# Optimization experiments

Hardware: AMD Instinct MI355X
Metric: run time of the kernel (lower is better)

Reference implementation:

```python
import jax, jax.numpy as jnp
import numpy as np

N_HEADS = 16
EMBED_DIM = 1024
HEAD_DIM = EMBED_DIM // N_HEADS
SRC_LEN = 128  # diagonal offset of the tril mask
B, T = 2, 2048


def setup_inputs() -> dict:
    key = jax.random.key(0)
    ks = jax.random.split(key, 7)
    s = 0.02
    return {
        "x": jax.random.normal(ks[0], (B, T, EMBED_DIM), dtype=jnp.float32),
        "Wq": jax.random.normal(ks[1], (EMBED_DIM, EMBED_DIM), dtype=jnp.float32) * s,
        "bq": jax.random.normal(ks[2], (EMBED_DIM,), dtype=jnp.float32) * s,
        "Wk": jax.random.normal(ks[3], (EMBED_DIM, EMBED_DIM), dtype=jnp.float32) * s,
        "bk": jax.random.normal(ks[4], (EMBED_DIM,), dtype=jnp.float32) * s,
        "Wv": jax.random.normal(ks[5], (EMBED_DIM, EMBED_DIM), dtype=jnp.float32) * s,
        "bv": jax.random.normal(ks[6], (EMBED_DIM,), dtype=jnp.float32) * s,
    }


def reference(x, Wq, bq, Wk, bk, Wv, bv):
    b, t, c = x.shape
    # project and split heads: [B, H, T, Dh]
    def heads(w, bias):
        y = x @ w.T + bias
        return y.reshape(b, t, N_HEADS, HEAD_DIM).transpose(0, 2, 1, 3)

    q = heads(Wq, bq)
    k = heads(Wk, bk)
    v = heads(Wv, bv)

    scale = HEAD_DIM ** -0.5
    attn = jnp.einsum("bhqd,bhkd->bhqk", q, k) * scale  # [B,H,T,T]
    # prefix-causal mask: key j allowed iff j <= i + SRC_LEN
    i = jnp.arange(t)[:, None]
    j = jnp.arange(t)[None, :]
    mask = j <= i + SRC_LEN  # [T, T]
    attn = jnp.where(mask[None, None], attn, -jnp.inf)
    attn = jax.nn.softmax(attn, axis=-1)
    # dropout p=0.0 -> identity in eval/reference
    out = jnp.einsum("bhqk,bhkd->bhqd", attn, v)  # [B,H,T,Dh]
    return out.transpose(0, 2, 1, 3).reshape(b, t, c)
```

## Files before the change

### kernel.cpp

```cpp
#include <hip/hip_runtime.h>
#include <hip/hip_bf16.h>

#define B_    2
#define T_    2048
#define C_    1024
#define H_    16
#define D_    64
#define SRCL_ 128

typedef short  short8 __attribute__((ext_vector_type(8)));
typedef float  f32x4  __attribute__((ext_vector_type(4)));
typedef unsigned short ushort4_t __attribute__((ext_vector_type(4)));

#define QSCALE 0.18033688011112042f

__device__ inline unsigned short f2bf(float f) {
    union { float f; unsigned u; } v; v.f = f;
    unsigned r = v.u + 0x7FFFu + ((v.u >> 16) & 1u);
    return (unsigned short)(r >> 16);
}

#if __has_builtin(__builtin_amdgcn_exp2f)
#define EXP2F(x) __builtin_amdgcn_exp2f(x)
#else
#define EXP2F(x) exp2f(x)
#endif

__device__ __forceinline__ void async_ld16(const void* g, void* l) {
    __builtin_amdgcn_global_load_lds(
        (const __attribute__((address_space(1))) unsigned int*)g,
        (__attribute__((address_space(3))) unsigned int*)l, 16, 0, 0);
}

__global__ __launch_bounds__(256) void convert_all(
        const float* __restrict__ x,
        const float* __restrict__ wq,
        const float* __restrict__ wk,
        const float* __restrict__ wv,
        unsigned short* __restrict__ xb,
        unsigned short* __restrict__ wb)
{
    const int NX = (B_ * T_ * C_) / 4;
    const int NW = (C_ * C_) / 4;
    int i = blockIdx.x * 256 + threadIdx.x;
    const float4* src;
    ushort4_t* dst;
    if (i < NX)               { src = (const float4*)x;  dst = (ushort4_t*)xb;                }
    else if (i < NX + NW)     { src = (const float4*)wq; dst = (ushort4_t*)wb;                i -= NX; }
    else if (i < NX + 2*NW)   { src = (const float4*)wk; dst = (ushort4_t*)(wb + C_*C_);      i -= NX + NW; }
    else                      { src = (const float4*)wv; dst = (ushort4_t*)(wb + 2*C_*C_);    i -= NX + 2*NW; }
    float4 v = src[i];
    ushort4_t o;
    o.x = f2bf(v.x); o.y = f2bf(v.y); o.z = f2bf(v.z); o.w = f2bf(v.w);
    dst[i] = o;
}

__global__ __launch_bounds__(256, 4) void gemm_qkv(
        const unsigned short* __restrict__ xb,
        const unsigned short* __restrict__ wb,
        const float* __restrict__ bq,
        const float* __restrict__ bk,
        const float* __restrict__ bv,
        unsigned short* __restrict__ qo,
        unsigned short* __restrict__ kt,
        unsigned short* __restrict__ vt)
{
    __shared__ __align__(16) unsigned short uni[16640];

    const int tid  = threadIdx.x;
    const int wave = tid >> 6;
    const int lane = tid & 63;
    const int lane15 = lane & 15;
    const int quad   = lane >> 4;
    const int wm = wave >> 1;
    const int wn = wave & 1;
    const int m0 = (blockIdx.x & 31) * 128;
    const int n0 = (blockIdx.x >> 5) * 128;

    f32x4 acc[4][4];
#pragma unroll
    for (int mi = 0; mi < 4; ++mi)
#pragma unroll
        for (int ni = 0; ni < 4; ++ni)
            acc[mi][ni] = (f32x4){0.f, 0.f, 0.f, 0.f};

    const int c0   = wave * 2;
    const int rowi0 = 16 * c0 + (lane >> 2);
    const int rowi1 = 16 * (c0 + 1) + (lane >> 2);
    const int col8 = (lane & 3) * 8;

    const unsigned short* xrow0 = &xb[(m0 + rowi0) * 1024 + col8];
    const unsigned short* xrow1 = &xb[(m0 + rowi1) * 1024 + col8];
    const unsigned short* wrow0 = &wb[(n0 + rowi0) * 1024 + col8];
    const unsigned short* wrow1 = &wb[(n0 + rowi1) * 1024 + col8];

    async_ld16(xrow0, &uni[c0 * 512]);
    async_ld16(xrow1, &uni[(c0 + 1) * 512]);
    async_ld16(wrow0, &uni[4096 + c0 * 512]);
    async_ld16(wrow1, &uni[4096 + (c0 + 1) * 512]);

    for (int it = 0; it < 32; ++it) {
        __asm__ volatile("s_waitcnt vmcnt(0)\n\ts_barrier" ::: "memory");

        if (it + 1 < 32) {
            const int k1 = (it + 1) * 32;
            unsigned short* nb = &uni[((it + 1) & 1) * 8192];
            async_ld16(xrow0 + k1, &nb[c0 * 512]);
            async_ld16(xrow1 + k1, &nb[(c0 + 1) * 512]);
            async_ld16(wrow0 + k1, &nb[4096 + c0 * 512]);
            async_ld16(wrow1 + k1, &nb[4096 + (c0 + 1) * 512]);
        }

        const unsigned short* As = &uni[(it & 1) * 8192];
        const unsigned short* Bs = As + 4096;

        short8 a[4], bf[4];
#pragma unroll
        for (int mi = 0; mi < 4; ++mi)
            a[mi] = *(const short8*)&As[(wm * 64 + mi * 16 + lane15) * 32 + quad * 8];
#pragma unroll
        for (int ni = 0; ni < 4; ++ni)
            bf[ni] = *(const short8*)&Bs[(wn * 64 + ni * 16 + lane15) * 32 + quad * 8];
#pragma unroll
        for (int mi = 0; mi < 4; ++mi)
#pragma unroll
            for (int ni = 0; ni < 4; ++ni)
                acc[mi][ni] = __builtin_amdgcn_mfma_f32_16x16x32_bf16(a[mi], bf[ni], acc[mi][ni], 0, 0, 0);
    }

    __syncthreads();

    const int colbase = n0 + wn * 64;
    const int which   = colbase >> 10;
    const int jj0     = colbase & 1023;
    const int h       = jj0 >> 6;
    const int rowbase = m0 + wm * 64;
    const int bidx    = rowbase >> 11;
    const int t0      = rowbase & 2047;
    const size_t bh   = (size_t)bidx * H_ + h;
    const float* bias_p = (which == 0 ? bq : (which == 1 ? bk : bv)) + jj0;
    const float oscale  = (which == 0) ? QSCALE : 1.0f;

    unsigned short* stage = &uni[wave * 4160];

    if (which != 2) {
#pragma unroll
        for (int ni = 0; ni < 4; ++ni) {
            const float bias = bias_p[ni * 16 + lane15];
            const int d = ni * 16 + lane15;
            const int dbase = (d >> 3) * 520 + (d & 7);
#pragma unroll
            for (int mi = 0; mi < 4; ++mi)
#pragma unroll
                for (int r = 0; r < 4; ++r) {
                    const int tt = mi * 16 + quad * 4 + r;
                    stage[dbase + tt * 8] = f2bf((acc[mi][ni][r] + bias) * oscale);
                }
        }
    } else {
#pragma unroll
        for (int ni = 0; ni < 4; ++ni) {
            const float bias = bias_p[ni * 16 + lane15];
            const int d = ni * 16 + lane15;
#pragma unroll
            for (int mi = 0; mi < 4; ++mi)
#pragma unroll
                for (int r = 0; r < 4; ++r) {
                    const int tt = mi * 16 + quad * 4 + r;
                    stage[(tt >> 3) * 520 + d * 8 + (tt & 7)] = f2bf(acc[mi][ni][r] + bias);
                }
        }
    }

    unsigned short* gdst =
        (which == 0 ? qo : (which == 1 ? kt : vt)) + bh * (size_t)(T_ * D_) + (t0 >> 6) * 4096;

#pragma unroll
    for (int c = 0; c < 8; ++c) {
        *(short8*)&gdst[(c * 64 + lane) * 8] = *(const short8*)&stage[c * 520 + lane * 8];
    }
}

__global__ __launch_bounds__(256, 3) void attn(
        const unsigned short* __restrict__ qg,
        const unsigned short* __restrict__ kg,
        const unsigned short* __restrict__ vg,
        float* __restrict__ out)
{
    __shared__ __align__(16) unsigned short stage[2][8192];
    __shared__ __align__(16) unsigned short Ps[4][16 * 88];

    const int tid  = threadIdx.x;
    const int wave = tid >> 6;
    const int lane = tid & 63;
    const int lane15 = lane & 15;
    const int quad   = lane >> 4;

    const int bh = blockIdx.x & 31;
    const int a  = 31 - (blockIdx.x >> 5);
    const int b  = bh >> 4;
    const int h  = bh & 15;
    const int i0 = a * 64 + wave * 16;

    const unsigned short* Q  = qg + (size_t)bh * T_ * D_;
    const unsigned short* KT = kg + (size_t)bh * T_ * D_;
    const unsigned short* VT = vg + (size_t)bh * T_ * D_;

    const int qrow = wave * 16 + lane15;
    const short8 qf0 = *(const short8*)&Q[a * 4096 + quad * 512 + qrow * 8];
    const short8 qf1 = *(const short8*)&Q[a * 4096 + (4 + quad) * 512 + qrow * 8];

    f32x4 o_acc[4];
#pragma unroll
    for (int di = 0; di < 4; ++di) o_acc[di] = (f32x4){0.f, 0.f, 0.f, 0.f};
    float l_p = 0.f;

    unsigned short* myPs = &Ps[wave][0];
    const int ntiles = min(a + 3, 32);
    const int limit  = i0 + lane15 + SRCL_;

    const int ib = wave * 4;
    const int loff = lane * 8;

#pragma unroll
    for (int c = 0; c < 4; ++c) {
        const int i = ib + c;
        const unsigned short* src = (i < 8) ? &KT[i * 512 + loff]
                                            : &VT[(i - 8) * 512 + loff];
        async_ld16(src, &stage[0][i * 512]);
    }

    for (int it = 0; it < ntiles; ++it) {
        __asm__ volatile("s_waitcnt vmcnt(0)\n\ts_barrier" ::: "memory");

        if (it + 1 < ntiles) {
            unsigned short* nb = &stage[(it + 1) & 1][0];
            const size_t tb = (size_t)(it + 1) * 4096;
#pragma unroll
            for (int c = 0; c < 4; ++c) {
                const int i = ib + c;
                const unsigned short* src = (i < 8) ? &KT[tb + i * 512 + loff]
                                                    : &VT[tb + (i - 8) * 512 + loff];
                async_ld16(src, &nb[i * 512]);
            }
        }

        const unsigned short* sb = &stage[it & 1][0];
        const int j0 = it << 6;

        f32x4 sv[4];
#pragma unroll
        for (int ni = 0; ni < 4; ++ni) {
            const short8 kf0 = *(const short8*)&sb[quad * 512 + (ni * 16 + lane15) * 8];
            const short8 kf1 = *(const short8*)&sb[(4 + quad) * 512 + (ni * 16 + lane15) * 8];
            f32x4 t = (f32x4){0.f, 0.f, 0.f, 0.f};
            t = __builtin_amdgcn_mfma_f32_16x16x32_bf16(kf0, qf0, t, 0, 0, 0);
            t = __builtin_amdgcn_mfma_f32_16x16x32_bf16(kf1, qf1, t, 0, 0, 0);
            sv[ni] = t;
        }

        if (j0 + 63 > i0 + SRCL_) {
#pragma unroll
            for (int ni = 0; ni < 4; ++ni)
#pragma unroll
                for (int r = 0; r < 4; ++r) {
                    const int key = j0 + ni * 16 + quad * 4 + r;
                    if (key > limit) sv[ni][r] = -INFINITY;
                }
        }

        float lacc = 0.f;
#pragma unroll
        for (int ni = 0; ni < 4; ++ni) {
            const float p0 = EXP2F(sv[ni][0]);
            const float p1 = EXP2F(sv[ni][1]);
            const float p2 = EXP2F(sv[ni][2]);
            const float p3 = EXP2F(sv[ni][3]);
            lacc += (p0 + p1) + (p2 + p3);
            const unsigned u0 = __float_as_uint(p0) + 0x8000u;
            const unsigned u1 = __float_as_uint(p1) + 0x8000u;
            const unsigned u2 = __float_as_uint(p2) + 0x8000u;
            const unsigned u3 = __float_as_uint(p3) + 0x8000u;
            uint2 w;
            w.x = __builtin_amdgcn_perm(u1, u0, 0x07060302);
            w.y = __builtin_amdgcn_perm(u3, u2, 0x07060302);
            *(uint2*)&myPs[lane15 * 88 + ni * 16 + quad * 4] = w;
        }
        l_p += lacc;

        const short8 pf0 = *(const short8*)&myPs[lane15 * 88 + quad * 8];
        const short8 pf1 = *(const short8*)&myPs[lane15 * 88 + 32 + quad * 8];

#pragma unroll
        for (int di = 0; di < 4; ++di) {
            const short8 vf0 = *(const short8*)&sb[4096 + quad * 512 + (di * 16 + lane15) * 8];
            const short8 vf1 = *(const short8*)&sb[4096 + (4 + quad) * 512 + (di * 16 + lane15) * 8];
            o_acc[di] = __builtin_amdgcn_mfma_f32_16x16x32_bf16(vf0, pf0, o_acc[di], 0, 0, 0);
            o_acc[di] = __builtin_amdgcn_mfma_f32_16x16x32_bf16(vf1, pf1, o_acc[di], 0, 0, 0);
        }
    }

    __syncthreads();

    float l0s = l_p + __shfl_xor(l_p, 16);
    const float inv = 1.0f / (l0s + __shfl_xor(l0s, 32));

    float* myOs = (float*)&stage[0][0] + wave * 2048;
#pragma unroll
    for (int di = 0; di < 4; ++di) {
        f32x4 v = o_acc[di] * inv;
        *(f32x4*)&myOs[lane15 * 68 + di * 16 + quad * 4] = v;
    }
    float* orow0 = out + ((size_t)(b * T_ + i0)) * C_ + h * 64;
#pragma unroll
    for (int c = 0; c < 4; ++c) {
        const int idx = c * 64 + lane;
        const int t   = idx >> 4;
        const int dc  = (idx & 15) * 4;
        float4 v = *(float4*)&myOs[t * 68 + dc];
        *(float4*)(orow0 + (size_t)t * C_ + dc) = v;
    }
}

extern "C" void kernel_launch(void* const* d_in, const int* in_sizes, int n_in,
                              void* d_out, int out_size, void* d_ws, size_t ws_size,
                              hipStream_t stream) {
    const float* x  = (const float*)d_in[0];
    const float* Wq = (const float*)d_in[1];
    const float* bq = (const float*)d_in[2];
    const float* Wk = (const float*)d_in[3];
    const float* bk = (const float*)d_in[4];
    const float* Wv = (const float*)d_in[5];
    const float* bv = (const float*)d_in[6];
    float* out = (float*)d_out;

    unsigned short* xb  = (unsigned short*)d_ws;
    unsigned short* wb  = xb  + (size_t)B_ * T_ * C_;
    unsigned short* qb  = wb  + (size_t)3 * C_ * C_;
    unsigned short* ktb = qb  + (size_t)B_ * H_ * T_ * D_;
    unsigned short* vtb = ktb + (size_t)B_ * H_ * T_ * D_;

    convert_all<<<7168, 256, 0, stream>>>(x, Wq, Wk, Wv, xb, wb);
    gemm_qkv<<<768, 256, 0, stream>>>(xb, wb, bq, bk, bv, qb, ktb, vtb);
    attn<<<1024, 256, 0, stream>>>(qb, ktb, vtb, out);
}
```

Baseline: 148.8 us.

## Split attention key tiles across waves instead of query rows, reduce partial outputs

Each wave now handles a 16-key slice of every 64-key tile for all 64 query rows, instead of 16 query rows over all keys. This lets P stay in registers as the B operand of 16x16x16 MFMAs and removes the per-tile LDS round trip for P. The cost is four times more output accumulators per wave, which raises register pressure, plus a multi-barrier cross-wave reduction of O and the row sums at the end. The PV step now uses the smaller 16x16x16 MFMA, issued more often, and its fallback path silently returns the accumulator unchanged if the builtin is missing.

```diff
diff --git a/kernel.cpp b/kernel.cpp
--- a/kernel.cpp
+++ b/kernel.cpp
@@ -9,6 +9,7 @@
 #define SRCL_ 128
 
 typedef short  short8 __attribute__((ext_vector_type(8)));
+typedef short  short4_t __attribute__((ext_vector_type(4)));
 typedef float  f32x4  __attribute__((ext_vector_type(4)));
 typedef unsigned short ushort4_t __attribute__((ext_vector_type(4)));
 
@@ -25,6 +26,17 @@
 #else
 #define EXP2F(x) exp2f(x)
 #endif
+
+__device__ __forceinline__ f32x4 mfma16_bf16(short4_t a, short4_t b, f32x4 c) {
+#if __has_builtin(__builtin_amdgcn_mfma_f32_16x16x16bf16_1k)
+    return __builtin_amdgcn_mfma_f32_16x16x16bf16_1k(a, b, c, 0, 0, 0);
+#elif __has_builtin(__builtin_amdgcn_mfma_f32_16x16x16_bf16)
+    return __builtin_amdgcn_mfma_f32_16x16x16_bf16(a, b, c, 0, 0, 0);
+#else
+    (void)a; (void)b;
+    return c;
+#endif
+}
 
 __device__ __forceinline__ void async_ld16(const void* g, void* l) {
     __builtin_amdgcn_global_load_lds(
@@ -188,10 +200,10 @@
         float* __restrict__ out)
 {
     __shared__ __align__(16) unsigned short stage[2][8192];
-    __shared__ __align__(16) unsigned short Ps[4][16 * 88];
+    __shared__ float Lb[4][4][16];
 
     const int tid  = threadIdx.x;
-    const int wave = tid >> 6;
+    const int s    = tid >> 6;
     const int lane = tid & 63;
     const int lane15 = lane & 15;
     const int quad   = lane >> 4;
@@ -200,26 +212,29 @@
     const int a  = 31 - (blockIdx.x >> 5);
     const int b  = bh >> 4;
     const int h  = bh & 15;
-    const int i0 = a * 64 + wave * 16;
 
     const unsigned short* Q  = qg + (size_t)bh * T_ * D_;
     const unsigned short* KT = kg + (size_t)bh * T_ * D_;
     const unsigned short* VT = vg + (size_t)bh * T_ * D_;
 
-    const int qrow = wave * 16 + lane15;
-    const short8 qf0 = *(const short8*)&Q[a * 4096 + quad * 512 + qrow * 8];
-    const short8 qf1 = *(const short8*)&Q[a * 4096 + (4 + quad) * 512 + qrow * 8];
-
-    f32x4 o_acc[4];
-#pragma unroll
-    for (int di = 0; di < 4; ++di) o_acc[di] = (f32x4){0.f, 0.f, 0.f, 0.f};
-    float l_p = 0.f;
-
-    unsigned short* myPs = &Ps[wave][0];
+    short8 qf[4][2];
+#pragma unroll
+    for (int nq = 0; nq < 4; ++nq) {
+        const int row = nq * 16 + lane15;
+        qf[nq][0] = *(const short8*)&Q[a * 4096 + quad * 512 + row * 8];
+        qf[nq][1] = *(const short8*)&Q[a * 4096 + (4 + quad) * 512 + row * 8];
+    }
+
+    f32x4 o_acc[4][4];
+#pragma unroll
+    for (int dd = 0; dd < 4; ++dd)
+#pragma unroll
+        for (int nq = 0; nq < 4; ++nq)
+            o_acc[dd][nq] = (f32x4){0.f, 0.f, 0.f, 0.f};
+    float l_part[4] = {0.f, 0.f, 0.f, 0.f};
+
     const int ntiles = min(a + 3, 32);
-    const int limit  = i0 + lane15 + SRCL_;
-
-    const int ib = wave * 4;
+    const int ib = s * 4;
     const int loff = lane * 8;
 
 #pragma unroll
@@ -246,79 +261,145 @@
         }
 
         const unsigned short* sb = &stage[it & 1][0];
-        const int j0 = it << 6;
+
+        const int krow = s * 16 + lane15;
+        const short8 kf0 = *(const short8*)&sb[quad * 512 + krow * 8];
+        const short8 kf1 = *(const short8*)&sb[(4 + quad) * 512 + krow * 8];
+
+        short4_t vf[4];
+        {
+            const int tkey = s * 16 + quad * 4;
+            const int ct   = tkey >> 3;
+            const int t7   = tkey & 7;
+#pragma unroll
+            for (int dd = 0; dd < 4; ++dd) {
+                const int d = dd * 16 + lane15;
+                vf[dd] = *(const short4_t*)&sb[4096 + ct * 512 + d * 8 + t7];
+            }
+        }
 
         f32x4 sv[4];
 #pragma unroll
-        for (int ni = 0; ni < 4; ++ni) {
-            const short8 kf0 = *(const short8*)&sb[quad * 512 + (ni * 16 + lane15) * 8];
-            const short8 kf1 = *(const short8*)&sb[(4 + quad) * 512 + (ni * 16 + lane15) * 8];
+        for (int nq = 0; nq < 4; ++nq) {
             f32x4 t = (f32x4){0.f, 0.f, 0.f, 0.f};
-            t = __builtin_amdgcn_mfma_f32_16x16x32_bf16(kf0, qf0, t, 0, 0, 0);
-            t = __builtin_amdgcn_mfma_f32_16x16x32_bf16(kf1, qf1, t, 0, 0, 0);
-            sv[ni] = t;
-        }
-
-        if (j0 + 63 > i0 + SRCL_) {
-#pragma unroll
-            for (int ni = 0; ni < 4; ++ni)
-#pragma unroll
-                for (int r = 0; r < 4; ++r) {
-                    const int key = j0 + ni * 16 + quad * 4 + r;
-                    if (key > limit) sv[ni][r] = -INFINITY;
-                }
-        }
-
-        float lacc = 0.f;
-#pragma unroll
-        for (int ni = 0; ni < 4; ++ni) {
-            const float p0 = EXP2F(sv[ni][0]);
-            const float p1 = EXP2F(sv[ni][1]);
-            const float p2 = EXP2F(sv[ni][2]);
-            const float p3 = EXP2F(sv[ni][3]);
-            lacc += (p0 + p1) + (p2 + p3);
+            t = __builtin_amdgcn_mfma_f32_16x16x32_bf16(kf0, qf[nq][0], t, 0, 0, 0);
+            t = __builtin_amdgcn_mfma_f32_16x16x32_bf16(kf1, qf[nq][1], t, 0, 0, 0);
+            sv[nq] = t;
+        }
+
+        if (it == a + 2) {
+            const int keyb = it * 64 + s * 16 + quad * 4;
+#pragma unroll
+            for (int nq = 0; nq < 4; ++nq) {
+                const int limit = a * 64 + nq * 16 + lane15 + SRCL_;
+#pragma unroll
+                for (int r = 0; r < 4; ++r)
+                    if (keyb + r > limit) sv[nq][r] = -INFINITY;
+            }
+        }
+
+        short4_t pf[4];
+#pragma unroll
+        for (int nq = 0; nq < 4; ++nq) {
+            const float p0 = EXP2F(sv[nq][0]);
+            const float p1 = EXP2F(sv[nq][1]);
+            const float p2 = EXP2F(sv[nq][2]);
+            const float p3 = EXP2F(sv[nq][3]);
+            l_part[nq] += (p0 + p1) + (p2 + p3);
             const unsigned u0 = __float_as_uint(p0) + 0x8000u;
             const unsigned u1 = __float_as_uint(p1) + 0x8000u;
             const unsigned u2 = __float_as_uint(p2) + 0x8000u;
             const unsigned u3 = __float_as_uint(p3) + 0x8000u;
-            uint2 w;
-            w.x = __builtin_amdgcn_perm(u1, u0, 0x07060302);
-            w.y = __builtin_amdgcn_perm(u3, u2, 0x07060302);
-            *(uint2*)&myPs[lane15 * 88 + ni * 16 + quad * 4] = w;
-        }
-        l_p += lacc;
-
-        const short8 pf0 = *(const short8*)&myPs[lane15 * 88 + quad * 8];
-        const short8 pf1 = *(const short8*)&myPs[lane15 * 88 + 32 + quad * 8];
-
-#pragma unroll
-        for (int di = 0; di < 4; ++di) {
-            const short8 vf0 = *(const short8*)&sb[4096 + quad * 512 + (di * 16 + lane15) * 8];
-            const short8 vf1 = *(const short8*)&sb[4096 + (4 + quad) * 512 + (di * 16 + lane15) * 8];
-            o_acc[di] = __builtin_amdgcn_mfma_f32_16x16x32_bf16(vf0, pf0, o_acc[di], 0, 0, 0);
-            o_acc[di] = __builtin_amdgcn_mfma_f32_16x16x32_bf16(vf1, pf1, o_acc[di], 0, 0, 0);
-        }
-    }
-
+            union { uint2 u; short4_t s4; } pk;
+            pk.u.x = __builtin_amdgcn_perm(u1, u0, 0x07060302);
+            pk.u.y = __builtin_amdgcn_perm(u3, u2, 0x07060302);
+            pf[nq] = pk.s4;
+        }
+
+#pragma unroll
+        for (int dd = 0; dd < 4; ++dd)
+#pragma unroll
+            for (int nq = 0; nq < 4; ++nq)
+                o_acc[dd][nq] = mfma16_bf16(vf[dd], pf[nq], o_acc[dd][nq]);
+    }
+
+#pragma unroll
+    for (int nq = 0; nq < 4; ++nq) {
+        float v = l_part[nq];
+        v += __shfl_xor(v, 16);
+        v += __shfl_xor(v, 32);
+        l_part[nq] = v;
+    }
+    if (lane < 16) {
+#pragma unroll
+        for (int nq = 0; nq < 4; ++nq) Lb[s][nq][lane] = l_part[nq];
+    }
     __syncthreads();
 
-    float l0s = l_p + __shfl_xor(l_p, 16);
-    const float inv = 1.0f / (l0s + __shfl_xor(l0s, 32));
-
-    float* myOs = (float*)&stage[0][0] + wave * 2048;
-#pragma unroll
-    for (int di = 0; di < 4; ++di) {
-        f32x4 v = o_acc[di] * inv;
-        *(f32x4*)&myOs[lane15 * 68 + di * 16 + quad * 4] = v;
-    }
-    float* orow0 = out + ((size_t)(b * T_ + i0)) * C_ + h * 64;
-#pragma unroll
-    for (int c = 0; c < 4; ++c) {
-        const int idx = c * 64 + lane;
-        const int t   = idx >> 4;
-        const int dc  = (idx & 15) * 4;
-        float4 v = *(float4*)&myOs[t * 68 + dc];
-        *(float4*)(orow0 + (size_t)t * C_ + dc) = v;
+    float inv[4];
+#pragma unroll
+    for (int nq = 0; nq < 4; ++nq)
+        inv[nq] = 1.0f / (Lb[0][nq][lane15] + Lb[1][nq][lane15] +
+                          Lb[2][nq][lane15] + Lb[3][nq][lane15]);
+
+    float* Mf0 = (float*)&stage[0][0];
+    float* Mf1 = Mf0 + 64 * 36;
+
+#pragma unroll
+    for (int dh = 0; dh < 2; ++dh) {
+        if (s == 1 || s == 3) {
+            float* Mf = (s == 1) ? Mf0 : Mf1;
+#pragma unroll
+            for (int c = 0; c < 2; ++c)
+#pragma unroll
+                for (int nq = 0; nq < 4; ++nq)
+                    *(f32x4*)&Mf[(nq * 16 + lane15) * 36 + c * 16 + quad * 4] =
+                        o_acc[dh * 2 + c][nq];
+        }
+        __syncthreads();
+        if (s == 0 || s == 2) {
+            const float* Mf = (s == 0) ? Mf0 : Mf1;
+#pragma unroll
+            for (int c = 0; c < 2; ++c)
+#pragma unroll
+                for (int nq = 0; nq < 4; ++nq)
+                    o_acc[dh * 2 + c][nq] +=
+                        *(const f32x4*)&Mf[(nq * 16 + lane15) * 36 + c * 16 + quad * 4];
+        }
+        __syncthreads();
+        if (s == 2) {
+#pragma unroll
+            for (int c = 0; c < 2; ++c)
+#pragma unroll
+                for (int nq = 0; nq < 4; ++nq)
+                    *(f32x4*)&Mf0[(nq * 16 + lane15) * 36 + c * 16 + quad * 4] =
+                        o_acc[dh * 2 + c][nq];
+        }
+        __syncthreads();
+        if (s == 0) {
+#pragma unroll
+            for (int c = 0; c < 2; ++c)
+#pragma unroll
+                for (int nq = 0; nq < 4; ++nq) {
+                    f32x4 v = o_acc[dh * 2 + c][nq] +
+                        *(const f32x4*)&Mf0[(nq * 16 + lane15) * 36 + c * 16 + quad * 4];
+                    v *= inv[nq];
+                    *(f32x4*)&Mf1[(nq * 16 + lane15) * 36 + c * 16 + quad * 4] = v;
+                }
+        }
+        __syncthreads();
+        {
+            float* orow = out + ((size_t)(b * T_ + a * 64 + s * 16)) * C_ + h * 64 + dh * 32;
+#pragma unroll
+            for (int c = 0; c < 2; ++c) {
+                const int idx = c * 64 + lane;
+                const int tl  = idx >> 3;
+                const int dc  = (idx & 7) * 4;
+                float4 v = *(float4*)&Mf1[(s * 16 + tl) * 36 + dc];
+                *(float4*)(orow + (size_t)tl * C_ + dc) = v;
+            }
+        }
+        __syncthreads();
     }
 }
 
```

Result: no change. 149.6 us (+0.5%).
